# Optimization experiments

Hardware: AMD Instinct MI355X
Metric: run time of the kernel (lower is better)

Reference implementation:

```python
import jax, jax.numpy as jnp
import numpy as np


def grid_sample_3d(vol, grid, align_corners=False):
    """PyTorch-equivalent 5D grid_sample, trilinear, padding_mode='zeros'.
    vol: [N,C,D,H,W]; grid: [N,Do,Ho,Wo,3] with last dim (x,y,z) in normalized coords.
    """
    N, C, D, H, W = vol.shape

    def unnorm(c, s):
        s = jnp.asarray(s, vol.dtype)
        if align_corners:
            return (c + 1.0) * (s - 1.0) * 0.5
        return ((c + 1.0) * s - 1.0) * 0.5

    ix = unnorm(grid[..., 0], W)  # [N,Do,Ho,Wo]
    iy = unnorm(grid[..., 1], H)
    iz = unnorm(grid[..., 2], D)

    def sample_one(vn, ix, iy, iz):
        # vn: [C,D,H,W]; ix/iy/iz: [Do,Ho,Wo]
        x0 = jnp.floor(ix); y0 = jnp.floor(iy); z0 = jnp.floor(iz)
        tx = ix - x0; ty = iy - y0; tz = iz - z0

        def corner(dz, dy, dx):
            zc = z0 + dz; yc = y0 + dy; xc = x0 + dx
            w = (tz if dz else 1.0 - tz) * (ty if dy else 1.0 - ty) * (tx if dx else 1.0 - tx)
            inb = (zc >= 0) & (zc < D) & (yc >= 0) & (yc < H) & (xc >= 0) & (xc < W)
            zi = jnp.clip(zc, 0, D - 1).astype(jnp.int32)
            yi = jnp.clip(yc, 0, H - 1).astype(jnp.int32)
            xi = jnp.clip(xc, 0, W - 1).astype(jnp.int32)
            v = vn[:, zi, yi, xi]  # [C,Do,Ho,Wo]
            return v * (w * inb.astype(vn.dtype))[None]

        acc = corner(0, 0, 0)
        for dz in (0, 1):
            for dy in (0, 1):
                for dx in (0, 1):
                    if (dz, dy, dx) != (0, 0, 0):
                        acc = acc + corner(dz, dy, dx)
        return acc

    return jax.vmap(sample_one)(vol, ix, iy, iz)


def _to_sample_grid(locs_chfirst):
    # [N,3,D,H,W] channel order (z_idx,y_idx,x_idx) -> [N,D,H,W,3] (x,y,z)
    return jnp.moveaxis(locs_chfirst, 1, -1)[..., ::-1]


def setup_inputs() -> dict:
    key = jax.random.key(0)
    k0, k1, k2 = jax.random.split(key, 3)
    D, H, W = 160, 192, 160
    src = jax.random.normal(k0, (1, 1, D, H, W), jnp.float32)
    flow1 = jax.random.normal(k1, (1, 3, D, H, W), jnp.float32) * 5.0
    flow2 = jax.random.normal(k2, (1, 3, D, H, W), jnp.float32) * 5.0
    vs = [jnp.arange(s, dtype=jnp.float32) for s in (D, H, W)]
    grid = jnp.stack(jnp.meshgrid(*vs, indexing='ij'))[None]  # [1,3,D,H,W]
    range_flow = jnp.float32(0.4)
    return {"src": src, "flow1": flow1, "flow2": flow2, "grid": grid, "range_flow": range_flow}


def reference(src, flow1, flow2, grid, range_flow):
    D, H, W = flow1.shape[2:]
    # normalization 2*(c/(s-1)-0.5) per spatial channel (align_corners=True convention,
    # but grid_sample is called with torch's default align_corners=False -> replicate)
    scales = jnp.array([D - 1, H - 1, W - 1], jnp.float32).reshape(1, 3, 1, 1, 1)

    # (deform_1_img from flow1 alone is computed in the original but never returned)

    # warp flow1 by flow2 -- NOTE: the original passes UNNORMALIZED voxel coords here
    grid2 = grid + flow2 * range_flow  # [1,3,D,H,W]
    flow1_warped = grid_sample_3d(flow1, _to_sample_grid(grid2), align_corners=False)
    out_flow = flow1_warped + flow2

    new_locs_total = grid + out_flow * range_flow
    new_locs_total = 2.0 * (new_locs_total / scales - 0.5)
    deform_2_img = grid_sample_3d(src, _to_sample_grid(new_locs_total), align_corners=False)
    return (deform_2_img, out_flow)
```

## Files before the change

### kernel.cpp

```cpp
#include <hip/hip_runtime.h>

#define DD 160
#define HH 192
#define WW 160
constexpr int DHW = DD * HH * WW;

typedef float vfloat4 __attribute__((ext_vector_type(4)));

__device__ __forceinline__ float sample_src(const float* __restrict__ src,
                                            float sz, float sy, float sx) {
    float zf = floorf(sz), yf = floorf(sy), xf = floorf(sx);
    int z0 = (int)zf, y0 = (int)yf, x0 = (int)xf;
    float tz = sz - zf, ty = sy - yf, tx = sx - xf;

    float wz[2] = {1.0f - tz, tz};
    float wy[2] = {1.0f - ty, ty};
    float wx[2] = {1.0f - tx, tx};
    int zi[2], yi[2], xi[2];
    #pragma unroll
    for (int d = 0; d < 2; ++d) {
        int zc = z0 + d, yc = y0 + d, xc = x0 + d;
        if (zc < 0 || zc >= DD) wz[d] = 0.0f;
        if (yc < 0 || yc >= HH) wy[d] = 0.0f;
        if (xc < 0 || xc >= WW) wx[d] = 0.0f;
        zi[d] = min(max(zc, 0), DD - 1);
        yi[d] = min(max(yc, 0), HH - 1);
        xi[d] = min(max(xc, 0), WW - 1);
    }
    float v[8];
    #pragma unroll
    for (int dz = 0; dz < 2; ++dz)
        #pragma unroll
        for (int dy = 0; dy < 2; ++dy) {
            int rowoff = (zi[dz] * HH + yi[dy]) * WW;
            #pragma unroll
            for (int dx = 0; dx < 2; ++dx)
                v[dz * 4 + dy * 2 + dx] = src[rowoff + xi[dx]];
        }
    float acc = 0.0f;
    #pragma unroll
    for (int dz = 0; dz < 2; ++dz)
        #pragma unroll
        for (int dy = 0; dy < 2; ++dy)
            #pragma unroll
            for (int dx = 0; dx < 2; ++dx)
                acc += wz[dz] * wy[dy] * wx[dx] * v[dz * 4 + dy * 2 + dx];
    return acc;
}

__global__ __launch_bounds__(256) void st_fused_kernel(
    const float* __restrict__ src,
    const float* __restrict__ flow1,
    const float* __restrict__ flow2,
    const float* __restrict__ prf,
    float* __restrict__ out)
{
    int tid = blockIdx.x * 256 + threadIdx.x;
    int idx0 = tid * 4;
    if (idx0 >= DHW) return;

    const float rf = prf[0];

    int xb = idx0 % WW;
    int t = idx0 / WW;
    int y = t % HH;
    int z = t / HH;

    const vfloat4 f2zv = *(const vfloat4*)(flow2 + idx0);
    const vfloat4 f2yv = *(const vfloat4*)(flow2 + idx0 + DHW);
    const vfloat4 f2xv = *(const vfloat4*)(flow2 + idx0 + 2 * DHW);

    vfloat4 sval, vofz, vofy, vofx;

    #pragma unroll
    for (int j = 0; j < 4; ++j) {
        int x = xb + j;
        float f2z = f2zv[j], f2y = f2yv[j], f2x = f2xv[j];

        float g2z = (float)z + f2z * rf;
        float g2y = (float)y + f2y * rf;
        float g2x = (float)x + f2x * rf;
        float iz = ((g2z + 1.0f) * (float)DD - 1.0f) * 0.5f;
        float iy = ((g2y + 1.0f) * (float)HH - 1.0f) * 0.5f;
        float ix = ((g2x + 1.0f) * (float)WW - 1.0f) * 0.5f;

        float fwz = 0.0f, fwy = 0.0f, fwx = 0.0f;
        if (ix > -1.0f && ix < (float)WW &&
            iy > -1.0f && iy < (float)HH &&
            iz > -1.0f && iz < (float)DD) {
            float zf = floorf(iz), yf = floorf(iy), xf = floorf(ix);
            int z0 = (int)zf, y0 = (int)yf, x0 = (int)xf;
            float tz = iz - zf, ty = iy - yf, tx = ix - xf;
            #pragma unroll
            for (int dz = 0; dz < 2; ++dz) {
                int zc = z0 + dz;
                if (zc < 0 || zc >= DD) continue;
                float wz = dz ? tz : 1.0f - tz;
                #pragma unroll
                for (int dy = 0; dy < 2; ++dy) {
                    int yc = y0 + dy;
                    if (yc < 0 || yc >= HH) continue;
                    float wzy = wz * (dy ? ty : 1.0f - ty);
                    #pragma unroll
                    for (int dx = 0; dx < 2; ++dx) {
                        int xc = x0 + dx;
                        if (xc < 0 || xc >= WW) continue;
                        float w = wzy * (dx ? tx : 1.0f - tx);
                        int off = (zc * HH + yc) * WW + xc;
                        fwz += w * flow1[off];
                        fwy += w * flow1[off + DHW];
                        fwx += w * flow1[off + 2 * DHW];
                    }
                }
            }
        }

        float ofz = fwz + f2z;
        float ofy = fwy + f2y;
        float ofx = fwx + f2x;
        vofz[j] = ofz; vofy[j] = ofy; vofx[j] = ofx;

        float nz = (float)z + ofz * rf;
        float ny = (float)y + ofy * rf;
        float nx = (float)x + ofx * rf;
        float cz = 2.0f * (nz / (float)(DD - 1) - 0.5f);
        float cy = 2.0f * (ny / (float)(HH - 1) - 0.5f);
        float cx = 2.0f * (nx / (float)(WW - 1) - 0.5f);
        float sz2 = ((cz + 1.0f) * (float)DD - 1.0f) * 0.5f;
        float sy2 = ((cy + 1.0f) * (float)HH - 1.0f) * 0.5f;
        float sx2 = ((cx + 1.0f) * (float)WW - 1.0f) * 0.5f;

        sval[j] = sample_src(src, sz2, sy2, sx2);
    }

    __builtin_nontemporal_store(sval, (vfloat4*)(out + idx0));
    __builtin_nontemporal_store(vofz, (vfloat4*)(out + DHW + idx0));
    __builtin_nontemporal_store(vofy, (vfloat4*)(out + 2 * DHW + idx0));
    __builtin_nontemporal_store(vofx, (vfloat4*)(out + 3 * DHW + idx0));
}

extern "C" void kernel_launch(void* const* d_in, const int* in_sizes, int n_in,
                              void* d_out, int out_size, void* d_ws, size_t ws_size,
                              hipStream_t stream) {
    const float* src   = (const float*)d_in[0];
    const float* flow1 = (const float*)d_in[1];
    const float* flow2 = (const float*)d_in[2];
    const float* prf   = (const float*)d_in[4];
    float* out = (float*)d_out;

    int threads_total = DHW / 4;
    int blocks = (threads_total + 255) / 256;
    st_fused_kernel<<<blocks, 256, 0, stream>>>(src, flow1, flow2, prf, out);
}
```

Before: 263.4 us.

## Batch src gathers across four voxels, swizzle block order, nontemporal flow2 loads

Splits the per-voxel loop into phases: first compute all flow1 trilinear samples for four voxels, then compute every src corner index, then issue all 32 src gathers together before accumulating with FMAs. This is meant to expose more memory-level parallelism and hide gather latency. It also remaps block IDs with an XCD-style swizzle (groups of 8) so contiguous blocks share an L2, and reads flow2 with nontemporal loads. The cost is higher register pressure, which may lower occupancy.

After: 265.6 us. No clear change (+0.8%).

```diff
diff --git a/kernel.cpp b/kernel.cpp
--- a/kernel.cpp
+++ b/kernel.cpp
@@ -7,47 +7,6 @@
 
 typedef float vfloat4 __attribute__((ext_vector_type(4)));
 
-__device__ __forceinline__ float sample_src(const float* __restrict__ src,
-                                            float sz, float sy, float sx) {
-    float zf = floorf(sz), yf = floorf(sy), xf = floorf(sx);
-    int z0 = (int)zf, y0 = (int)yf, x0 = (int)xf;
-    float tz = sz - zf, ty = sy - yf, tx = sx - xf;
-
-    float wz[2] = {1.0f - tz, tz};
-    float wy[2] = {1.0f - ty, ty};
-    float wx[2] = {1.0f - tx, tx};
-    int zi[2], yi[2], xi[2];
-    #pragma unroll
-    for (int d = 0; d < 2; ++d) {
-        int zc = z0 + d, yc = y0 + d, xc = x0 + d;
-        if (zc < 0 || zc >= DD) wz[d] = 0.0f;
-        if (yc < 0 || yc >= HH) wy[d] = 0.0f;
-        if (xc < 0 || xc >= WW) wx[d] = 0.0f;
-        zi[d] = min(max(zc, 0), DD - 1);
-        yi[d] = min(max(yc, 0), HH - 1);
-        xi[d] = min(max(xc, 0), WW - 1);
-    }
-    float v[8];
-    #pragma unroll
-    for (int dz = 0; dz < 2; ++dz)
-        #pragma unroll
-        for (int dy = 0; dy < 2; ++dy) {
-            int rowoff = (zi[dz] * HH + yi[dy]) * WW;
-            #pragma unroll
-            for (int dx = 0; dx < 2; ++dx)
-                v[dz * 4 + dy * 2 + dx] = src[rowoff + xi[dx]];
-        }
-    float acc = 0.0f;
-    #pragma unroll
-    for (int dz = 0; dz < 2; ++dz)
-        #pragma unroll
-        for (int dy = 0; dy < 2; ++dy)
-            #pragma unroll
-            for (int dx = 0; dx < 2; ++dx)
-                acc += wz[dz] * wy[dy] * wx[dx] * v[dz * 4 + dy * 2 + dx];
-    return acc;
-}
-
 __global__ __launch_bounds__(256) void st_fused_kernel(
     const float* __restrict__ src,
     const float* __restrict__ flow1,
@@ -55,36 +14,39 @@
     const float* __restrict__ prf,
     float* __restrict__ out)
 {
-    int tid = blockIdx.x * 256 + threadIdx.x;
+    int bid = (int)blockIdx.x;
+    int nb  = (int)gridDim.x;
+    int swz = bid;
+    if ((nb & 7) == 0) {
+        int chunk = nb >> 3;
+        swz = (bid & 7) * chunk + (bid >> 3);
+    }
+    int tid  = swz * 256 + (int)threadIdx.x;
     int idx0 = tid * 4;
     if (idx0 >= DHW) return;
 
     const float rf = prf[0];
 
     int xb = idx0 % WW;
-    int t = idx0 / WW;
-    int y = t % HH;
-    int z = t / HH;
+    int t  = idx0 / WW;
+    int y  = t % HH;
+    int z  = t / HH;
 
-    const vfloat4 f2zv = *(const vfloat4*)(flow2 + idx0);
-    const vfloat4 f2yv = *(const vfloat4*)(flow2 + idx0 + DHW);
-    const vfloat4 f2xv = *(const vfloat4*)(flow2 + idx0 + 2 * DHW);
+    const vfloat4 f2zv = __builtin_nontemporal_load((const vfloat4*)(flow2 + idx0));
+    const vfloat4 f2yv = __builtin_nontemporal_load((const vfloat4*)(flow2 + idx0 + DHW));
+    const vfloat4 f2xv = __builtin_nontemporal_load((const vfloat4*)(flow2 + idx0 + 2 * DHW));
 
-    vfloat4 sval, vofz, vofy, vofx;
-
+    float fwz[4], fwy[4], fwx[4];
     #pragma unroll
     for (int j = 0; j < 4; ++j) {
+        fwz[j] = 0.0f; fwy[j] = 0.0f; fwx[j] = 0.0f;
         int x = xb + j;
-        float f2z = f2zv[j], f2y = f2yv[j], f2x = f2xv[j];
-
-        float g2z = (float)z + f2z * rf;
-        float g2y = (float)y + f2y * rf;
-        float g2x = (float)x + f2x * rf;
+        float g2z = (float)z + f2zv[j] * rf;
+        float g2y = (float)y + f2yv[j] * rf;
+        float g2x = (float)x + f2xv[j] * rf;
         float iz = ((g2z + 1.0f) * (float)DD - 1.0f) * 0.5f;
         float iy = ((g2y + 1.0f) * (float)HH - 1.0f) * 0.5f;
         float ix = ((g2x + 1.0f) * (float)WW - 1.0f) * 0.5f;
-
-        float fwz = 0.0f, fwy = 0.0f, fwx = 0.0f;
         if (ix > -1.0f && ix < (float)WW &&
             iy > -1.0f && iy < (float)HH &&
             iz > -1.0f && iz < (float)DD) {
@@ -107,17 +69,26 @@
                         if (xc < 0 || xc >= WW) continue;
                         float w = wzy * (dx ? tx : 1.0f - tx);
                         int off = (zc * HH + yc) * WW + xc;
-                        fwz += w * flow1[off];
-                        fwy += w * flow1[off + DHW];
-                        fwx += w * flow1[off + 2 * DHW];
+                        fwz[j] += w * flow1[off];
+                        fwy[j] += w * flow1[off + DHW];
+                        fwx[j] += w * flow1[off + 2 * DHW];
                     }
                 }
             }
         }
+    }
 
-        float ofz = fwz + f2z;
-        float ofy = fwy + f2y;
-        float ofx = fwx + f2x;
+    vfloat4 vofz, vofy, vofx;
+    float wz[4][2], wy[4][2], wx[4][2];
+    int   ro[4][2][2];
+    int   xic[4][2];
+
+    #pragma unroll
+    for (int j = 0; j < 4; ++j) {
+        int x = xb + j;
+        float ofz = fwz[j] + f2zv[j];
+        float ofy = fwy[j] + f2yv[j];
+        float ofx = fwx[j] + f2xv[j];
         vofz[j] = ofz; vofy[j] = ofy; vofx[j] = ofx;
 
         float nz = (float)z + ofz * rf;
@@ -130,7 +101,56 @@
         float sy2 = ((cy + 1.0f) * (float)HH - 1.0f) * 0.5f;
         float sx2 = ((cx + 1.0f) * (float)WW - 1.0f) * 0.5f;
 
-        sval[j] = sample_src(src, sz2, sy2, sx2);
+        float zf = floorf(sz2), yf = floorf(sy2), xf = floorf(sx2);
+        int z0 = (int)zf, y0 = (int)yf, x0 = (int)xf;
+        float tz = sz2 - zf, ty = sy2 - yf, tx = sx2 - xf;
+
+        wz[j][0] = 1.0f - tz; wz[j][1] = tz;
+        wy[j][0] = 1.0f - ty; wy[j][1] = ty;
+        wx[j][0] = 1.0f - tx; wx[j][1] = tx;
+
+        int zi[2], yi[2];
+        #pragma unroll
+        for (int d = 0; d < 2; ++d) {
+            int zc = z0 + d, yc = y0 + d, xc = x0 + d;
+            if (zc < 0 || zc >= DD) wz[j][d] = 0.0f;
+            if (yc < 0 || yc >= HH) wy[j][d] = 0.0f;
+            if (xc < 0 || xc >= WW) wx[j][d] = 0.0f;
+            zi[d]     = min(max(zc, 0), DD - 1);
+            yi[d]     = min(max(yc, 0), HH - 1);
+            xic[j][d] = min(max(xc, 0), WW - 1);
+        }
+        #pragma unroll
+        for (int dz = 0; dz < 2; ++dz)
+            #pragma unroll
+            for (int dy = 0; dy < 2; ++dy)
+                ro[j][dz][dy] = (zi[dz] * HH + yi[dy]) * WW;
+    }
+
+    float v[4][8];
+    #pragma unroll
+    for (int j = 0; j < 4; ++j)
+        #pragma unroll
+        for (int dz = 0; dz < 2; ++dz)
+            #pragma unroll
+            for (int dy = 0; dy < 2; ++dy)
+                #pragma unroll
+                for (int dx = 0; dx < 2; ++dx)
+                    v[j][dz * 4 + dy * 2 + dx] = src[ro[j][dz][dy] + xic[j][dx]];
+
+    vfloat4 sval;
+    #pragma unroll
+    for (int j = 0; j < 4; ++j) {
+        float acc = 0.0f;
+        #pragma unroll
+        for (int dz = 0; dz < 2; ++dz)
+            #pragma unroll
+            for (int dy = 0; dy < 2; ++dy)
+                #pragma unroll
+                for (int dx = 0; dx < 2; ++dx)
+                    acc = fmaf(wz[j][dz] * wy[j][dy] * wx[j][dx],
+                               v[j][dz * 4 + dy * 2 + dx], acc);
+        sval[j] = acc;
     }
 
     __builtin_nontemporal_store(sval, (vfloat4*)(out + idx0));
```
